# Kernel optimization log

Measured on AMD Instinct MI355X. Metric: run time of the kernel, lower is better.

The kernel has to match this reference:

```python
import jax, jax.numpy as jnp
import numpy as np

EPS = 1e-5
NUM_HEADS = 8
TOP_K = 4

def _ln(x, s, b):
    m = x.mean(-1, keepdims=True)
    v = ((x - m) ** 2).mean(-1, keepdims=True)
    return (x - m) / jnp.sqrt(v + EPS) * s + b

def _mha(x, wq, bq, wk, bk, wv, bv, wo, bo):
    B, S, D = x.shape
    dh = D // NUM_HEADS
    q = (x @ wq + bq).reshape(B, S, NUM_HEADS, dh)
    k = (x @ wk + bk).reshape(B, S, NUM_HEADS, dh)
    v = (x @ wv + bv).reshape(B, S, NUM_HEADS, dh)
    att = jnp.einsum('bqhd,bkhd->bhqk', q, k) / np.sqrt(dh).astype(x.dtype)
    a = jax.nn.softmax(att, axis=-1)
    o = jnp.einsum('bhqk,bkhd->bqhd', a, v).reshape(B, S, D)
    return o @ wo + bo

def _moe(x, rd, ru, w1, b1, w2, b2, ws1, bs1, ws2, bs2):
    B, S, D = x.shape
    N = B * S
    E = ru.shape[-1]
    t = x.reshape(N, D)
    scores = (t @ rd) @ ru                       # [N,E] low-rank router
    probs = jax.nn.softmax(scores, axis=-1)
    tv, ti = jax.lax.top_k(probs, TOP_K)          # [N,K]
    tw = tv / tv.sum(-1, keepdims=True)           # renormalized gate weights
    oh = jax.nn.one_hot(ti, E, dtype=t.dtype)     # [N,K,E]
    gates = (oh * tw[..., None]).sum(1)           # sparse [N,E] combine weights
    h = jax.nn.gelu(jnp.einsum('nd,edh->enh', t, w1) + b1[:, None, :])
    eo = jnp.einsum('enh,ehd->end', h, w2) + b2[:, None, :]
    routed = jnp.einsum('end,ne->nd', eo, gates)
    shared = jax.nn.gelu(t @ ws1 + bs1) @ ws2 + bs2
    out = (routed + shared).reshape(B, S, D)
    # aux losses: load-balance + router z-loss
    f = oh.sum(1).mean(0)                         # mean assignments per expert
    P = probs.mean(0)
    lb = (E / TOP_K) * jnp.sum(f * P)
    z = jnp.mean(jax.nn.logsumexp(scores, axis=-1) ** 2)
    return out, lb, z

def reference(x, ln1_s, ln1_b, ln2_s, ln2_b, wq, bq, wk, bk, wv, bv, wo, bo,
              router_down, router_up, w1, b1, w2, b2, ws1, bs1, ws2, bs2, fn_s, fn_b):
    L = wq.shape[0]
    lbs, zs = [], []
    for l in range(L):
        x = x + _mha(_ln(x, ln1_s[l], ln1_b[l]), wq[l], bq[l], wk[l], bk[l],
                     wv[l], bv[l], wo[l], bo[l])
        moe_out, lb, z = _moe(_ln(x, ln2_s[l], ln2_b[l]), router_down[l], router_up[l],
                              w1[l], b1[l], w2[l], b2[l], ws1[l], bs1[l], ws2[l], bs2[l])
        x = x + moe_out
        lbs.append(lb)
        zs.append(z)
    x = _ln(x, fn_s, fn_b)
    return x, jnp.stack(lbs), jnp.stack(zs)

def setup_inputs() -> dict:
    key = jax.random.key(0)
    ks = jax.random.split(key, 16)
    L, D, E, R, H, HS, B, S = 2, 512, 32, 64, 512, 4096, 4, 1024
    w = 0.02  # init scale for weights
    return {
        'x': jax.random.normal(ks[0], (B, S, D), jnp.float32),
        'ln1_s': jnp.ones((L, D)), 'ln1_b': jnp.zeros((L, D)),
        'ln2_s': jnp.ones((L, D)), 'ln2_b': jnp.zeros((L, D)),
        'wq': jax.random.normal(ks[1], (L, D, D)) * w, 'bq': jnp.zeros((L, D)),
        'wk': jax.random.normal(ks[2], (L, D, D)) * w, 'bk': jnp.zeros((L, D)),
        'wv': jax.random.normal(ks[3], (L, D, D)) * w, 'bv': jnp.zeros((L, D)),
        'wo': jax.random.normal(ks[4], (L, D, D)) * w, 'bo': jnp.zeros((L, D)),
        'router_down': jax.random.normal(ks[5], (L, D, R)) * w,
        'router_up': jax.random.normal(ks[6], (L, R, E)) * w,
        'w1': jax.random.normal(ks[7], (L, E, D, H)) * w, 'b1': jnp.zeros((L, E, H)),
        'w2': jax.random.normal(ks[8], (L, E, H, D)) * w, 'b2': jnp.zeros((L, E, D)),
        'ws1': jax.random.normal(ks[9], (L, D, HS)) * w, 'bs1': jnp.zeros((L, HS)),
        'ws2': jax.random.normal(ks[10], (L, HS, D)) * w, 'bs2': jnp.zeros((L, D)),
        'fn_s': jnp.ones((D,)), 'fn_b': jnp.zeros((D,)),
    }
```

## Files before the change

### kernel.cpp

```cpp
#include <hip/hip_runtime.h>
#include <math.h>

#define NTOK    4096
#define DMODEL  512
#define NEXP    32
#define RRANK   64
#define HEXP    512
#define HSHARED 4096
#define SEQ     1024
#define BATCH   4
#define NHEAD   8
#define TOPK    4
#define NLAYER  2
#define QBLK    64
#define KBLK    64
#define MAXTILE 160
#define DDU     262144

typedef __attribute__((ext_vector_type(8))) short bf16x8;
typedef __attribute__((ext_vector_type(4))) float f32x4;

__device__ __forceinline__ float gelu_f(float x) {
    float t = tanhf(0.7978845608028654f * (x + 0.044715f * x * x * x));
    return 0.5f * x * (1.f + t);
}
__device__ __forceinline__ unsigned short f2bf(float f) {
    unsigned int u = __float_as_uint(f);
    u += 0x7FFFu + ((u >> 16) & 1u);
    return (unsigned short)(u >> 16);
}
__device__ __forceinline__ float bf2f(unsigned short u) {
    return __uint_as_float((unsigned int)u << 16);
}
__device__ __forceinline__ void gl_lds16(const void* g, void* l) {
    __builtin_amdgcn_global_load_lds(
        (const __attribute__((address_space(1))) void*)g,
        (__attribute__((address_space(3))) void*)l, 16, 0, 0);
}

__device__ __forceinline__ void ln_body(const float* x, const float* s, const float* b,
                                        unsigned short* outb, int rowblk) {
    int wave = threadIdx.x >> 6, lane = threadIdx.x & 63;
    int row = rowblk * 4 + wave;
    const float* xr = x + (size_t)row * DMODEL;
    float v[8];
    float sum = 0.f;
#pragma unroll
    for (int i = 0; i < 8; i++) { v[i] = xr[lane + i * 64]; sum += v[i]; }
#pragma unroll
    for (int o = 32; o; o >>= 1) sum += __shfl_xor(sum, o);
    float m = sum * (1.f / DMODEL);
    float vs = 0.f;
#pragma unroll
    for (int i = 0; i < 8; i++) { float d = v[i] - m; vs += d * d; }
#pragma unroll
    for (int o = 32; o; o >>= 1) vs += __shfl_xor(vs, o);
    float rstd = rsqrtf(vs * (1.f / DMODEL) + 1e-5f);
#pragma unroll
    for (int i = 0; i < 8; i++) {
        int c = lane + i * 64;
        outb[(size_t)row * DMODEL + c] = f2bf((v[i] - m) * rstd * s[c] + b[c]);
    }
}

template <int SK, bool MOE, int MODE, bool ROUTER = false>
__global__ __launch_bounds__(256) void reduceln_kernel(
    const float* __restrict__ pbuf, const float* __restrict__ bias,
    const unsigned short* __restrict__ eogb, const float* __restrict__ topw,
    const int* __restrict__ pos, float* __restrict__ xb,
    const float* __restrict__ s, const float* __restrict__ b,
    float* __restrict__ outf, unsigned short* __restrict__ outb,
    const float* __restrict__ rdru, float* __restrict__ rsc) {
    int wave = threadIdx.x >> 6, lane = threadIdx.x & 63;
    int row = blockIdx.x * 4 + wave;
    int cb = lane * 8;
    size_t base = (size_t)row * DMODEL + cb;
    float v[8];
    {
        float4 a0 = *(const float4*)(xb + base);
        float4 a1 = *(const float4*)(xb + base + 4);
        float4 b0 = *(const float4*)(bias + cb);
        float4 b1 = *(const float4*)(bias + cb + 4);
        v[0] = a0.x + b0.x; v[1] = a0.y + b0.y; v[2] = a0.z + b0.z; v[3] = a0.w + b0.w;
        v[4] = a1.x + b1.x; v[5] = a1.y + b1.y; v[6] = a1.z + b1.z; v[7] = a1.w + b1.w;
    }
#pragma unroll
    for (int sk = 0; sk < SK; sk++) {
        const float* p = pbuf + (size_t)sk * NTOK * DMODEL + base;
        float4 p0 = *(const float4*)p;
        float4 p1 = *(const float4*)(p + 4);
        v[0] += p0.x; v[1] += p0.y; v[2] += p0.z; v[3] += p0.w;
        v[4] += p1.x; v[5] += p1.y; v[6] += p1.z; v[7] += p1.w;
    }
    if (MOE) {
#pragma unroll
        for (int k = 0; k < TOPK; k++) {
            float w = topw[row * TOPK + k];
            bf16x8 e = *(const bf16x8*)(eogb + (size_t)pos[row * TOPK + k] * DMODEL + cb);
#pragma unroll
            for (int i = 0; i < 8; i++) v[i] += w * bf2f((unsigned short)e[i]);
        }
    }
    *(float4*)(xb + base) = make_float4(v[0], v[1], v[2], v[3]);
    *(float4*)(xb + base + 4) = make_float4(v[4], v[5], v[6], v[7]);
    float sum = 0.f;
#pragma unroll
    for (int i = 0; i < 8; i++) sum += v[i];
#pragma unroll
    for (int o = 32; o; o >>= 1) sum += __shfl_xor(sum, o);
    float m = sum * (1.f / DMODEL);
    float vs = 0.f;
#pragma unroll
    for (int i = 0; i < 8; i++) { float d = v[i] - m; vs += d * d; }
#pragma unroll
    for (int o = 32; o; o >>= 1) vs += __shfl_xor(vs, o);
    float rstd = rsqrtf(vs * (1.f / DMODEL) + 1e-5f);
    float rr[8];
#pragma unroll
    for (int i = 0; i < 8; i++) {
        int c = cb + i;
        rr[i] = (v[i] - m) * rstd * s[c] + b[c];
        if (MODE != 1) outf[(size_t)row * DMODEL + c] = rr[i];
        if (MODE != 0) outb[(size_t)row * DMODEL + c] = f2bf(rr[i]);
    }
    if (ROUTER) {
        float sc[NEXP];
#pragma unroll
        for (int e = 0; e < NEXP; e++) sc[e] = 0.f;
#pragma unroll
        for (int i = 0; i < 8; i++) {
            const float4* rp = (const float4*)(rdru + (size_t)(cb + i) * NEXP);
            float rv = rr[i];
#pragma unroll
            for (int e4 = 0; e4 < 8; e4++) {
                float4 q = rp[e4];
                sc[e4 * 4 + 0] += rv * q.x;
                sc[e4 * 4 + 1] += rv * q.y;
                sc[e4 * 4 + 2] += rv * q.z;
                sc[e4 * 4 + 3] += rv * q.w;
            }
        }
#pragma unroll
        for (int e = 0; e < NEXP; e++) {
#pragma unroll
            for (int o = 32; o; o >>= 1) sc[e] += __shfl_xor(sc[e], o);
        }
        if (lane == 0) {
            float* rp = rsc + (size_t)row * NEXP;
#pragma unroll
            for (int e = 0; e < NEXP; e++) rp[e] = sc[e];
        }
    }
}

__device__ __forceinline__ void wt_tile_body(char* ldsraw, const float* src,
                                             unsigned short* dst, int K, int N,
                                             int tx, int ty) {
    float (*tbuf)[68] = (float(*)[68])ldsraw;
    int tid = threadIdx.x;
    int k0 = ty * 64, n0 = tx * 64;
    int r = tid >> 2, cb4 = (tid & 3) * 4;
#pragma unroll
    for (int i = 0; i < 4; i++)
        *(float4*)&tbuf[r][cb4 + i * 16] = *(const float4*)(src + (size_t)(k0 + r) * N + n0 + cb4 + i * 16);
    __syncthreads();
    int g = tid & 7, nr = tid >> 3;
#pragma unroll
    for (int i = 0; i < 2; i++) {
        int n = nr + i * 32;
        bf16x8 v;
#pragma unroll
        for (int j = 0; j < 8; j++) v[j] = (short)f2bf(tbuf[g * 8 + j][n]);
        *(bf16x8*)(dst + (size_t)(n0 + n) * K + k0 + g * 8) = v;
    }
}

__device__ __forceinline__ void rdru_tile_body(char* ldsraw, const float* A,
                                               const float* W, float* C, int m0) {
    float (*Asf)[68] = (float(*)[68])ldsraw;
    float (*Wsf)[68] = (float(*)[68])(ldsraw + 4352);
    int tid = threadIdx.x;
    int ml = tid >> 2, kl = (tid & 3) << 2;
    const float* aptr = A + (size_t)(m0 + ml) * RRANK + kl;
    int kr = tid >> 4, nc = (tid & 15) << 2;
    bool wvalid = nc < NEXP;
    const float* wptr = W + (size_t)kr * NEXP + nc;
    int tm = (tid >> 4) << 2, tn = (tid & 15) << 2;
    float acc[4][4] = {{0.f}};
    for (int k0 = 0; k0 < RRANK; k0 += 16) {
        float4 av = *(const float4*)(aptr + k0);
        float4 wv = make_float4(0.f, 0.f, 0.f, 0.f);
        if (wvalid) wv = *(const float4*)(wptr + (size_t)k0 * NEXP);
        Asf[kl + 0][ml] = av.x; Asf[kl + 1][ml] = av.y;
        Asf[kl + 2][ml] = av.z; Asf[kl + 3][ml] = av.w;
        *(float4*)&Wsf[kr][nc] = wv;
        __syncthreads();
#pragma unroll
        for (int kk = 0; kk < 16; kk++) {
            float4 a4 = *(const float4*)&Asf[kk][tm];
            float4 w4 = *(const float4*)&Wsf[kk][tn];
            acc[0][0] += a4.x * w4.x; acc[0][1] += a4.x * w4.y; acc[0][2] += a4.x * w4.z; acc[0][3] += a4.x * w4.w;
            acc[1][0] += a4.y * w4.x; acc[1][1] += a4.y * w4.y; acc[1][2] += a4.y * w4.z; acc[1][3] += a4.y * w4.w;
            acc[2][0] += a4.z * w4.x; acc[2][1] += a4.z * w4.y; acc[2][2] += a4.z * w4.z; acc[2][3] += a4.z * w4.w;
            acc[3][0] += a4.w * w4.x; acc[3][1] += a4.w * w4.y; acc[3][2] += a4.w * w4.z; acc[3][3] += a4.w * w4.w;
        }
        __syncthreads();
    }
#pragma unroll
    for (int i = 0; i < 4; i++) {
        float* crow = C + (size_t)(m0 + tm + i) * NEXP;
#pragma unroll
        for (int j = 0; j < 4; j++) {
            int nn = tn + j;
            if (nn < NEXP) crow[nn] = acc[i][j];
        }
    }
}

__global__ __launch_bounds__(256) void prep0_kernel(
    const float* __restrict__ wq, const float* __restrict__ wk, const float* __restrict__ wv,
    const float* __restrict__ bq, const float* __restrict__ bk, const float* __restrict__ bv,
    unsigned short* __restrict__ wqkvt, float* __restrict__ bqkv, int* __restrict__ stats,
    const float* __restrict__ rdw, const float* __restrict__ ruw, float* __restrict__ rdru,
    const float* __restrict__ xb, const float* __restrict__ ln1_s, const float* __restrict__ ln1_b,
    unsigned short* __restrict__ hb) {
    __shared__ char lds[17408];
    int bkid = blockIdx.x;
    int tid = threadIdx.x;
    if (bkid < 192) {
        int w = bkid >> 6, t = bkid & 63;
        const float* src = (w == 0) ? wq : (w == 1 ? wk : wv);
        wt_tile_body(lds, src, wqkvt + (size_t)w * DDU, 512, 512, t & 7, t >> 3);
    } else if (bkid < 198) {
        int i = (bkid - 192) * 256 + tid;
        float val = (i < 512) ? bq[i] : (i < 1024 ? bk[i - 512] : bv[i - 1024]);
        bqkv[i] = val;
        if (i < 160) stats[i] = 0;
    } else if (bkid < 206) {
        rdru_tile_body(lds, rdw, ruw, rdru, (bkid - 198) * 64);
    } else {
        ln_body(xb, ln1_s, ln1_b, hb, bkid - 206);
    }
}

__global__ __launch_bounds__(256) void vtr_kernel(const unsigned short* __restrict__ QKV,
                                                  unsigned short* __restrict__ Vt) {
    int st = blockIdx.x, hh = blockIdx.y, bb = blockIdx.z;
    __shared__ unsigned short t[64][72];
    int r = threadIdx.x >> 3, g = threadIdx.x & 7;
#pragma unroll
    for (int i = 0; i < 2; i++) {
        int row = r + i * 32;
        bf16x8 v = *(const bf16x8*)(QKV + (size_t)(bb * SEQ + st * 64 + row) * 1536 + 1024 + hh * 64 + g * 8);
        *(bf16x8*)&t[row][g * 8] = v;
    }
    __syncthreads();
#pragma unroll
    for (int i = 0; i < 2; i++) {
        int d = r + i * 32;
        bf16x8 v;
#pragma unroll
        for (int j = 0; j < 8; j++) v[j] = (short)t[g * 8 + j][d];
        *(bf16x8*)(Vt + (size_t)((bb * NHEAD + hh) * 64 + d) * SEQ + st * 64 + g * 8) = v;
    }
}

template <bool GELU, bool GATHER, bool EXPERT, bool OUTBF16, int SK>
__device__ __forceinline__ void gemm_body(
    char* asb, char* bsb,
    unsigned int rb, unsigned int gx, unsigned int tot, int zidx,
    const unsigned short* Ab, const unsigned short* Wt,
    const float* bias, void* Cvoid, int M, int Nn, int Kk,
    const int* rowmap, const int* cntp, const int* offp, const int* tinfo) {
    constexpr int RS  = 128;
    constexpr int CH  = 8;
    constexpr int RPI = 8;
    constexpr int AIW = 4;
    constexpr int BIW = 2;
    unsigned int lg = (rb & 7) * (tot >> 3) + (rb >> 3);
    unsigned int bx = lg % gx;
    unsigned int by = lg / gx;
    int n0 = bx * 64;
    int m0;
    size_t cbase = 0;
    int kbeg = 0, kend = Kk;
    if (EXPERT) {
        int t = by;
        if (t >= tinfo[0]) return;
        int e = tinfo[1 + 2 * t];
        m0 = tinfo[2 + 2 * t];
        M = cntp[e];
        Wt += (size_t)e * Nn * Kk;
        bias += (size_t)e * Nn;
        int oe = offp[e];
        cbase = (size_t)oe * Nn;
        if (GATHER) rowmap += oe;
        else Ab += (size_t)oe * Kk;
    } else {
        m0 = by * 128;
    }
    if (SK > 1) {
        int chunk = Kk / SK;
        kbeg = zidx * chunk;
        kend = kbeg + chunk;
        cbase = (size_t)zidx * M * Nn;
    }
    int tid = threadIdx.x;
    int wave = tid >> 6, lane = tid & 63;
    int wm = wave >> 1, wn = wave & 1;
    int l15 = lane & 15, l16 = lane >> 4;
    int c16 = lane & (CH - 1);
    int ro  = lane / CH;

    const char* aptr[AIW];
    const char* bptr[BIW];
#pragma unroll
    for (int j = 0; j < AIW; j++) {
        int rloc = j * RPI + ro;
        int row = wave * 32 + rloc;
        int grow = m0 + row;
        int arow = GATHER ? rowmap[grow] : grow;
        int srcoff = ((c16 ^ (rloc & (CH - 1))) << 4);
        aptr[j] = (const char*)Ab + (((size_t)arow * Kk) << 1) + srcoff;
    }
#pragma unroll
    for (int j = 0; j < BIW; j++) {
        int rloc = j * RPI + ro;
        int row = wave * 16 + rloc;
        int srcoff = ((c16 ^ (rloc & (CH - 1))) << 4);
        bptr[j] = (const char*)Wt + (((size_t)(n0 + row) * Kk) << 1) + srcoff;
    }

    f32x4 acc[4][2];
#pragma unroll
    for (int m = 0; m < 4; m++)
#pragma unroll
        for (int n = 0; n < 2; n++)
#pragma unroll
            for (int j = 0; j < 4; j++) acc[m][n][j] = 0.f;

    for (int k0 = kbeg; k0 < kend; k0 += 64) {
        size_t kb = (size_t)k0 << 1;
#pragma unroll
        for (int j = 0; j < AIW; j++) gl_lds16(aptr[j] + kb, asb + wave * 32 * RS + j * 1024);
#pragma unroll
        for (int j = 0; j < BIW; j++) gl_lds16(bptr[j] + kb, bsb + wave * 16 * RS + j * 1024);
        __syncthreads();
#pragma unroll
        for (int kk = 0; kk < 2; kk++) {
            int k8 = kk * 4 + l16;
            bf16x8 a[4], b[2];
#pragma unroll
            for (int m = 0; m < 4; m++) {
                int row = wm * 64 + m * 16 + l15;
                a[m] = *(const bf16x8*)(asb + row * RS + ((k8 * 16) ^ ((row & (CH - 1)) << 4)));
            }
#pragma unroll
            for (int n = 0; n < 2; n++) {
                int row = wn * 32 + n * 16 + l15;
                b[n] = *(const bf16x8*)(bsb + row * RS + ((k8 * 16) ^ ((row & (CH - 1)) << 4)));
            }
#pragma unroll
            for (int m = 0; m < 4; m++)
#pragma unroll
                for (int n = 0; n < 2; n++)
                    acc[m][n] = __builtin_amdgcn_mfma_f32_16x16x32_bf16(a[m], b[n], acc[m][n], 0, 0, 0);
        }
        __syncthreads();
    }

#pragma unroll
    for (int m = 0; m < 4; m++) {
#pragma unroll
        for (int n = 0; n < 2; n++) {
            int col = n0 + wn * 32 + n * 16 + l15;
            float bv = (SK == 1 && bias) ? bias[col] : 0.f;
#pragma unroll
            for (int j = 0; j < 4; j++) {
                int row = m0 + wm * 64 + m * 16 + l16 * 4 + j;
                if (row >= M) continue;
                float val = acc[m][n][j] + bv;
                if (SK == 1 && GELU) val = gelu_f(val);
                if (SK == 1 && OUTBF16)
                    ((unsigned short*)Cvoid)[cbase + (size_t)row * Nn + col] = f2bf(val);
                else
                    ((float*)Cvoid)[cbase + (size_t)row * Nn + col] = val;
            }
        }
    }
}

template <int RIDER>
__global__ __launch_bounds__(256, 2) void qkv_kernel(
    const unsigned short* __restrict__ hb, const unsigned short* __restrict__ wqkvt,
    const float* __restrict__ bqkv, unsigned short* __restrict__ qkv_bf,
    const float* __restrict__ srcA, const float* __restrict__ srcB,
    unsigned short* __restrict__ dstA, unsigned short* __restrict__ dstB,
    int* __restrict__ stats) {
    __shared__ char lds[24576];
    unsigned int bid = blockIdx.x;
    if (bid < 768) {
        gemm_body<false, false, false, true, 1>(
            lds, lds + 16384, bid, 24, 768, 0,
            hb, wqkvt, bqkv, qkv_bf, NTOK, 1536, DMODEL, nullptr, nullptr, nullptr, nullptr);
    } else if (RIDER == 0) {
        int t = bid - 768;
        wt_tile_body(lds, srcA, dstA, 512, 512, t & 7, t >> 3);
    } else {
        unsigned int eb = bid - 768;
        if (eb < 2048) {
            int e = eb >> 6, tt = eb & 63;
            wt_tile_body(lds, srcA + (size_t)e * DDU, dstA + (size_t)e * DDU,
                         512, 512, tt & 7, tt >> 3);
        } else if (eb < 2560) {
            int t = eb - 2048;
            wt_tile_body(lds, srcB, dstB, 4096, 512, t & 7, t >> 3);
        } else {
            if (threadIdx.x < 160) stats[threadIdx.x] = 0;
        }
    }
}

__device__ __forceinline__ void attn_body(char* lds, unsigned int bid,
                                          const unsigned short* QKV,
                                          const unsigned short* Vt,
                                          unsigned short* O) {
    int qt = bid & 15, hh = (bid >> 4) & 7, bb = bid >> 7;
    char* Qs = lds;
    char* Ks = lds + 8192;
    char* Vs = lds + 16384;
    char* Ps = lds + 24576;
    int tid = threadIdx.x;
    int w = tid >> 6, l = tid & 63;
    int l15 = l & 15, l16 = l >> 4;

    {
        int r = tid >> 3, g = tid & 7;
        const unsigned short* qbase = QKV + (size_t)(bb * SEQ + qt * QBLK) * 1536 + hh * 64;
#pragma unroll
        for (int i = 0; i < 2; i++) {
            int row = r + i * 32;
            bf16x8 v = *(const bf16x8*)(qbase + (size_t)row * 1536 + g * 8);
            *(bf16x8*)(Qs + row * 128 + ((g * 16) ^ ((row & 7) << 4))) = v;
        }
    }
    f32x4 accO[4];
#pragma unroll
    for (int n = 0; n < 4; n++)
#pragma unroll
        for (int j = 0; j < 4; j++) accO[n][j] = 0.f;
    float m_r[4] = {-1e30f, -1e30f, -1e30f, -1e30f};
    float l_r[4] = {0.f, 0.f, 0.f, 0.f};

    const unsigned short* kbase = QKV + (size_t)(bb * SEQ) * 1536 + 512 + hh * 64;
    const unsigned short* vbase = Vt + (size_t)((bb * NHEAD + hh) * 64) * SEQ;

    for (int kt = 0; kt < SEQ / KBLK; kt++) {
        __syncthreads();
        {
            int r = tid >> 3, g = tid & 7;
#pragma unroll
            for (int i = 0; i < 2; i++) {
                int row = r + i * 32;
                bf16x8 kv = *(const bf16x8*)(kbase + (size_t)(kt * KBLK + row) * 1536 + g * 8);
                *(bf16x8*)(Ks + row * 128 + ((g * 16) ^ ((row & 7) << 4))) = kv;
                bf16x8 vv = *(const bf16x8*)(vbase + (size_t)row * SEQ + kt * KBLK + g * 8);
                *(bf16x8*)(Vs + row * 128 + ((g * 16) ^ ((row & 7) << 4))) = vv;
            }
        }
        __syncthreads();
        f32x4 s_acc[4];
#pragma unroll
        for (int n = 0; n < 4; n++)
#pragma unroll
            for (int j = 0; j < 4; j++) s_acc[n][j] = 0.f;
#pragma unroll
        for (int st = 0; st < 2; st++) {
            int kb = st * 64 + l16 * 16;
            int qrow = w * 16 + l15;
            bf16x8 a = *(const bf16x8*)(Qs + qrow * 128 + (kb ^ ((qrow & 7) << 4)));
#pragma unroll
            for (int n = 0; n < 4; n++) {
                int kr = n * 16 + l15;
                bf16x8 b = *(const bf16x8*)(Ks + kr * 128 + (kb ^ ((kr & 7) << 4)));
                s_acc[n] = __builtin_amdgcn_mfma_f32_16x16x32_bf16(a, b, s_acc[n], 0, 0, 0);
            }
        }
        char* pw = Ps + w * 2048;
#pragma unroll
        for (int j = 0; j < 4; j++) {
            float s0 = s_acc[0][j] * 0.125f, s1 = s_acc[1][j] * 0.125f;
            float s2 = s_acc[2][j] * 0.125f, s3 = s_acc[3][j] * 0.125f;
            float tmax = fmaxf(fmaxf(s0, s1), fmaxf(s2, s3));
#pragma unroll
            for (int o = 1; o < 16; o <<= 1) tmax = fmaxf(tmax, __shfl_xor(tmax, o));
            float mnew = fmaxf(m_r[j], tmax);
            float resc = __expf(m_r[j] - mnew);
            float p0 = __expf(s0 - mnew), p1 = __expf(s1 - mnew);
            float p2 = __expf(s2 - mnew), p3 = __expf(s3 - mnew);
            float ps = p0 + p1 + p2 + p3;
#pragma unroll
            for (int o = 1; o < 16; o <<= 1) ps += __shfl_xor(ps, o);
            l_r[j] = l_r[j] * resc + ps;
            m_r[j] = mnew;
            accO[0][j] *= resc; accO[1][j] *= resc;
            accO[2][j] *= resc; accO[3][j] *= resc;
            int prow = l16 * 4 + j;
            int sw = (prow & 7) << 4;
            *(unsigned short*)(pw + prow * 128 + ((2 * l15) ^ sw)) = f2bf(p0);
            *(unsigned short*)(pw + prow * 128 + ((2 * l15 + 32) ^ sw)) = f2bf(p1);
            *(unsigned short*)(pw + prow * 128 + ((2 * l15 + 64) ^ sw)) = f2bf(p2);
            *(unsigned short*)(pw + prow * 128 + ((2 * l15 + 96) ^ sw)) = f2bf(p3);
        }
#pragma unroll
        for (int st = 0; st < 2; st++) {
            int kb = st * 64 + l16 * 16;
            bf16x8 pa = *(const bf16x8*)(pw + l15 * 128 + (kb ^ ((l15 & 7) << 4)));
#pragma unroll
            for (int n = 0; n < 4; n++) {
                int vr = n * 16 + l15;
                bf16x8 vb = *(const bf16x8*)(Vs + vr * 128 + (kb ^ ((vr & 7) << 4)));
                accO[n] = __builtin_amdgcn_mfma_f32_16x16x32_bf16(pa, vb, accO[n], 0, 0, 0);
            }
        }
    }
    unsigned short* obase = O + (size_t)(bb * SEQ + qt * QBLK + w * 16) * DMODEL + hh * 64;
#pragma unroll
    for (int j = 0; j < 4; j++) {
        float inv = 1.f / l_r[j];
        int row = l16 * 4 + j;
#pragma unroll
        for (int n = 0; n < 4; n++)
            obase[(size_t)row * DMODEL + n * 16 + l15] = f2bf(accO[n][j] * inv);
    }
}

template <int RIDER>
__global__ __launch_bounds__(256, 2) void attn_kernel(
    const unsigned short* __restrict__ QKV, const unsigned short* __restrict__ Vt,
    unsigned short* __restrict__ O,
    const float* __restrict__ w1src, const float* __restrict__ ws1src,
    unsigned short* __restrict__ w1t, unsigned short* __restrict__ ws1t) {
    __shared__ char lds[32768];
    unsigned int bid = blockIdx.x;
    if (bid < 512) {
        attn_body(lds, bid, QKV, Vt, O);
    } else if (RIDER == 0) {
        unsigned int eb = bid - 512;
        if (eb < 2048) {
            int e = eb >> 6, tt = eb & 63;
            wt_tile_body(lds, w1src + (size_t)e * DDU, w1t + (size_t)e * DDU,
                         512, 512, tt & 7, tt >> 3);
        } else {
            int t = eb - 2048;
            wt_tile_body(lds, ws1src, ws1t, 512, 4096, t & 63, t >> 6);
        }
    }
}

template <int RIDER>
__global__ __launch_bounds__(256, 2) void op_kernel(
    const unsigned short* __restrict__ t1b, const unsigned short* __restrict__ wot,
    float* __restrict__ pbuf,
    const float* __restrict__ w2src, const float* __restrict__ ws2src,
    unsigned short* __restrict__ w2t, unsigned short* __restrict__ ws2t) {
    __shared__ char lds[24576];
    unsigned int bid = blockIdx.x;
    if (bid < 512) {
        gemm_body<false, false, false, false, 2>(
            lds, lds + 16384, bid & 255, 8, 256, bid >> 8,
            t1b, wot, nullptr, pbuf, NTOK, DMODEL, DMODEL, nullptr, nullptr, nullptr, nullptr);
    } else if (RIDER == 0) {
        unsigned int eb = bid - 512;
        if (eb < 2048) {
            int e = eb >> 6, tt = eb & 63;
            wt_tile_body(lds, w2src + (size_t)e * DDU, w2t + (size_t)e * DDU,
                         512, 512, tt & 7, tt >> 3);
        } else {
            int t = eb - 2048;
            wt_tile_body(lds, ws2src, ws2t, 4096, 512, t & 7, t >> 3);
        }
    }
}

__global__ __launch_bounds__(256, 2) void mlp1_kernel(
    const unsigned short* __restrict__ hb,
    const unsigned short* __restrict__ ws1t, const float* __restrict__ bs1,
    unsigned short* __restrict__ hidb,
    const unsigned short* __restrict__ w1t, const float* __restrict__ b1,
    unsigned short* __restrict__ ehid,
    const int* __restrict__ perm, const int* __restrict__ cnt,
    const int* __restrict__ poff, const int* __restrict__ tinfo,
    const float* __restrict__ nwq, const float* __restrict__ nwk,
    const float* __restrict__ nwv, const float* __restrict__ nwo,
    const float* __restrict__ nbq, const float* __restrict__ nbk, const float* __restrict__ nbv,
    unsigned short* __restrict__ wqkvt, unsigned short* __restrict__ wot,
    float* __restrict__ bqkv,
    const float* __restrict__ nrdw, const float* __restrict__ nruw, float* __restrict__ rdru) {
    __shared__ char lds[24576];
    unsigned int bid = blockIdx.x;
    if (bid < 2048) {
        gemm_body<true, false, false, true, 1>(
            lds, lds + 16384, bid, 64, 2048, 0,
            hb, ws1t, bs1, hidb, NTOK, HSHARED, DMODEL, nullptr, nullptr, nullptr, nullptr);
    } else if (bid < 3328) {
        gemm_body<true, true, true, true, 1>(
            lds, lds + 16384, bid - 2048, 8, 1280, 0,
            hb, w1t, b1, ehid, 0, HEXP, DMODEL, perm, cnt, poff, tinfo);
    } else {
        unsigned int eb = bid - 3328;
        if (eb < 256) {
            int w = eb >> 6, t = eb & 63;
            const float* src; unsigned short* dst;
            if (w == 0)      { src = nwq; dst = wqkvt; }
            else if (w == 1) { src = nwk; dst = wqkvt + DDU; }
            else if (w == 2) { src = nwv; dst = wqkvt + 2 * (size_t)DDU; }
            else             { src = nwo; dst = wot; }
            wt_tile_body(lds, src, dst, 512, 512, t & 7, t >> 3);
        } else if (eb < 262) {
            int i = (eb - 256) * 256 + threadIdx.x;
            float val = (i < 512) ? nbq[i] : (i < 1024 ? nbk[i - 512] : nbv[i - 1024]);
            bqkv[i] = val;
        } else {
            rdru_tile_body(lds, nrdw, nruw, rdru, (eb - 262) * 64);
        }
    }
}

__global__ __launch_bounds__(256, 2) void mlp2_kernel(
    const unsigned short* __restrict__ hidb,
    const unsigned short* __restrict__ ws2t, float* __restrict__ pbuf,
    const unsigned short* __restrict__ ehid,
    const unsigned short* __restrict__ w2t, const float* __restrict__ b2,
    unsigned short* __restrict__ eogb,
    const int* __restrict__ cnt, const int* __restrict__ poff,
    const int* __restrict__ tinfo,
    const float* __restrict__ nw1, const float* __restrict__ nws1,
    unsigned short* __restrict__ w1t, unsigned short* __restrict__ ws1t) {
    __shared__ char lds[24576];
    unsigned int bid = blockIdx.x;
    if (bid < 1024) {
        int zidx = bid >> 8;
        gemm_body<false, false, false, false, 4>(
            lds, lds + 16384, bid & 255, 8, 256, zidx,
            hidb, ws2t, nullptr, pbuf, NTOK, DMODEL, HSHARED, nullptr, nullptr, nullptr, nullptr);
    } else if (bid < 2304) {
        gemm_body<false, false, true, true, 1>(
            lds, lds + 16384, bid - 1024, 8, 1280, 0,
            ehid, w2t, b2, eogb, 0, DMODEL, HEXP, nullptr, cnt, poff, tinfo);
    } else {
        unsigned int eb = bid - 2304;
        if (eb < 2048) {
            int e = eb >> 6, tt = eb & 63;
            wt_tile_body(lds, nw1 + (size_t)e * DDU, w1t + (size_t)e * DDU,
                         512, 512, tt & 7, tt >> 3);
        } else {
            int t = eb - 2048;
            wt_tile_body(lds, nws1, ws1t, 512, 4096, t & 63, t >> 6);
        }
    }
}

__global__ __launch_bounds__(256) void router_topk(const float* __restrict__ rsc,
                                                   float* __restrict__ topw,
                                                   int* __restrict__ topi,
                                                   int* __restrict__ cnt,
                                                   float* __restrict__ sumP,
                                                   float* __restrict__ zacc) {
    __shared__ float wP[4][NEXP];
    __shared__ int wC[4][NEXP];
    __shared__ float wZ[4];
    int tid = threadIdx.x;
    int wv = tid >> 6, lane = tid & 63;
    int n = blockIdx.x * 256 + tid;
    float sc[NEXP];
    float mx = -1e30f;
#pragma unroll
    for (int e = 0; e < NEXP; e++) { sc[e] = rsc[n * NEXP + e]; mx = fmaxf(mx, sc[e]); }
    float se = 0.f;
#pragma unroll
    for (int e = 0; e < NEXP; e++) { sc[e] = expf(sc[e] - mx); se += sc[e]; }
    float invse = 1.f / se;
    float lse = mx + logf(se);
    float z = lse * lse;
#pragma unroll
    for (int o = 32; o; o >>= 1) z += __shfl_xor(z, o);
    if (lane == 0) wZ[wv] = z;
#pragma unroll
    for (int e = 0; e < NEXP; e++) {
        float pv = sc[e] * invse;
#pragma unroll
        for (int o = 32; o; o >>= 1) pv += __shfl_xor(pv, o);
        if (lane == 0) wP[wv][e] = pv;
    }
    float tv[TOPK]; int ti[TOPK];
#pragma unroll
    for (int k = 0; k < TOPK; k++) {
        float best = -1.f; int bi = 0;
#pragma unroll
        for (int e = 0; e < NEXP; e++) {
            if (sc[e] > best) { best = sc[e]; bi = e; }
        }
        tv[k] = best * invse; ti[k] = bi; sc[bi] = -1.f;
    }
    float s4 = tv[0] + tv[1] + tv[2] + tv[3];
#pragma unroll
    for (int k = 0; k < TOPK; k++) {
        topw[n * TOPK + k] = tv[k] / s4;
        topi[n * TOPK + k] = ti[k];
    }
#pragma unroll
    for (int e = 0; e < NEXP; e++) {
        unsigned long long b0 = __ballot(ti[0] == e);
        unsigned long long b1 = __ballot(ti[1] == e);
        unsigned long long b2 = __ballot(ti[2] == e);
        unsigned long long b3 = __ballot(ti[3] == e);
        if (lane == 0)
            wC[wv][e] = __popcll(b0) + __popcll(b1) + __popcll(b2) + __popcll(b3);
    }
    __syncthreads();
    if (tid < NEXP) {
        atomicAdd(&sumP[tid], wP[0][tid] + wP[1][tid] + wP[2][tid] + wP[3][tid]);
        atomicAdd(&cnt[tid], wC[0][tid] + wC[1][tid] + wC[2][tid] + wC[3][tid]);
    }
    if (tid == 0) atomicAdd(zacc, wZ[0] + wZ[1] + wZ[2] + wZ[3]);
}

__global__ void scanaux_kernel(const int* __restrict__ cnt, int* __restrict__ poff,
                               int* __restrict__ tinfo, int* __restrict__ perm,
                               const float* __restrict__ sumP, const float* __restrict__ zacc,
                               float* __restrict__ out_aux, int l) {
    int lane = threadIdx.x;
    int c = (lane < NEXP) ? cnt[lane] : 0;
    int nt = (c + 127) >> 7;
    int x = nt;
#pragma unroll
    for (int o = 1; o < 32; o <<= 1) {
        int y = __shfl_up(x, o);
        if (lane >= o) x += y;
    }
    int excl = x - nt;
    if (lane < NEXP) {
        poff[lane] = excl * 128;
        for (int i = 0; i < nt; i++) {
            tinfo[1 + 2 * (excl + i)] = lane;
            tinfo[2 + 2 * (excl + i)] = i * 128;
        }
        for (int i = c; i < nt * 128; i++) perm[excl * 128 + i] = 0;
    }
    float lb = (lane < NEXP) ? ((float)c / (float)NTOK) * (sumP[lane] / (float)NTOK) : 0.f;
#pragma unroll
    for (int o = 32; o; o >>= 1) lb += __shfl_xor(lb, o);
    if (lane == 31) {
        tinfo[0] = x;
        out_aux[l] = lb * (float)NEXP / (float)TOPK;
        out_aux[NLAYER + l] = zacc[0] / (float)NTOK;
    }
}

__global__ __launch_bounds__(256) void scatter_kernel(const int* __restrict__ topi,
                                                      const int* __restrict__ poff,
                                                      int* __restrict__ cursor,
                                                      int* __restrict__ perm,
                                                      int* __restrict__ pos) {
    __shared__ int lcnt[NEXP];
    __shared__ int lbase[NEXP];
    if (threadIdx.x < NEXP) lcnt[threadIdx.x] = 0;
    __syncthreads();
    int i = blockIdx.x * 256 + threadIdx.x;
    int e = topi[i];
    int lr = atomicAdd(&lcnt[e], 1);
    __syncthreads();
    if (threadIdx.x < NEXP && lcnt[threadIdx.x] > 0)
        lbase[threadIdx.x] = atomicAdd(&cursor[threadIdx.x], lcnt[threadIdx.x]);
    __syncthreads();
    int g = poff[e] + lbase[e] + lr;
    perm[g] = i >> 2;
    pos[i] = g;
}

extern "C" void kernel_launch(void* const* d_in, const int* in_sizes, int n_in,
                              void* d_out, int out_size, void* d_ws, size_t ws_size,
                              hipStream_t stream) {
    (void)in_sizes; (void)n_in; (void)out_size; (void)ws_size;
    const float* x_in  = (const float*)d_in[0];
    const float* ln1_s = (const float*)d_in[1];
    const float* ln1_b = (const float*)d_in[2];
    const float* ln2_s = (const float*)d_in[3];
    const float* ln2_b = (const float*)d_in[4];
    const float* wq = (const float*)d_in[5];
    const float* bq = (const float*)d_in[6];
    const float* wk = (const float*)d_in[7];
    const float* bk = (const float*)d_in[8];
    const float* wv = (const float*)d_in[9];
    const float* bv = (const float*)d_in[10];
    const float* wo = (const float*)d_in[11];
    const float* bo = (const float*)d_in[12];
    const float* rdw = (const float*)d_in[13];
    const float* ruw = (const float*)d_in[14];
    const float* w1 = (const float*)d_in[15];
    const float* b1 = (const float*)d_in[16];
    const float* w2 = (const float*)d_in[17];
    const float* b2 = (const float*)d_in[18];
    const float* ws1 = (const float*)d_in[19];
    const float* bs1 = (const float*)d_in[20];
    const float* ws2 = (const float*)d_in[21];
    const float* bs2 = (const float*)d_in[22];
    const float* fn_s = (const float*)d_in[23];
    const float* fn_b = (const float*)d_in[24];

    float* ws = (float*)d_ws;
    const size_t ND = (size_t)NTOK * DMODEL;
    const size_t PADROWS = (size_t)MAXTILE * 128;
    size_t o = 0;
    float* xb  = ws + o; o += ND;
    unsigned short* hb     = (unsigned short*)(ws + o); o += ND / 2;
    unsigned short* qkv_bf = (unsigned short*)(ws + o); o += (size_t)NTOK * 1536 / 2;
    unsigned short* vT     = (unsigned short*)(ws + o); o += ND / 2;
    unsigned short* t1b    = (unsigned short*)(ws + o); o += ND / 2;
    unsigned short* hidb   = (unsigned short*)(ws + o); o += (size_t)NTOK * HSHARED / 2;
    unsigned short* ehid   = (unsigned short*)(ws + o); o += PADROWS * HEXP / 2;
    unsigned short* eogb   = (unsigned short*)(ws + o); o += PADROWS * DMODEL / 2;
    float* pbuf = ws + o; o += 4 * ND;
    float* rdru = ws + o; o += (size_t)DMODEL * NEXP;
    float* rsc  = ws + o; o += (size_t)NTOK * NEXP;
    float* topw = ws + o; o += (size_t)NTOK * TOPK;
    float* bqkv = ws + o; o += 1536;
    int* topi = (int*)(ws + o); o += (size_t)NTOK * TOPK;
    int* pos  = (int*)(ws + o); o += (size_t)NTOK * TOPK;
    int* perm = (int*)(ws + o); o += PADROWS;
    int* stats = (int*)(ws + o); o += 256;
    int* tinfo = (int*)(ws + o); o += 512;
    int* cnt = stats;
    int* cursor = stats + 32;
    int* poff = stats + 64;
    float* sumP = (float*)(stats + 96);
    float* zacc = sumP + 32;
    unsigned short* wbf = (unsigned short*)(ws + o);
    unsigned short* wqkvt = wbf;
    unsigned short* wot  = wqkvt + 3 * (size_t)DDU;
    unsigned short* w1t  = wot + DDU;
    unsigned short* w2t  = w1t + (size_t)NEXP * DDU;
    unsigned short* ws1t = w2t + (size_t)NEXP * DDU;
    unsigned short* ws2t = ws1t + (size_t)DMODEL * HSHARED;

    float* out_x = (float*)d_out;
    float* out_aux = out_x + ND;

    hipMemcpyAsync(xb, x_in, ND * sizeof(float), hipMemcpyDeviceToDevice, stream);

    dim3 blk(256);

    for (int l = 0; l < NLAYER; l++) {
        const size_t DD = (size_t)DMODEL * DMODEL;
        bool hasNext = (l + 1 < NLAYER);
        int lnx = hasNext ? (l + 1) : l;
        if (l == 0) {
            prep0_kernel<<<1230, blk, 0, stream>>>(
                wq, wk, wv, bq, bk, bv, wqkvt, bqkv, stats,
                rdw, ruw, rdru, xb, ln1_s, ln1_b, hb);
            qkv_kernel<0><<<832, blk, 0, stream>>>(
                hb, wqkvt, bqkv, qkv_bf, wo, nullptr, wot, nullptr, nullptr);
        } else {
            qkv_kernel<1><<<3329, blk, 0, stream>>>(
                hb, wqkvt, bqkv, qkv_bf,
                w2 + (size_t)l * NEXP * DD, ws2 + (size_t)l * HSHARED * DMODEL,
                w2t, ws2t, stats);
        }
        vtr_kernel<<<dim3(SEQ / 64, NHEAD, BATCH), blk, 0, stream>>>(qkv_bf, vT);
        if (l == 0)
            attn_kernel<0><<<3072, blk, 0, stream>>>(qkv_bf, vT, t1b, w1, ws1, w1t, ws1t);
        else
            attn_kernel<1><<<512, blk, 0, stream>>>(qkv_bf, vT, t1b, nullptr, nullptr, nullptr, nullptr);
        if (l == 0)
            op_kernel<0><<<3072, blk, 0, stream>>>(t1b, wot, pbuf, w2, ws2, w2t, ws2t);
        else
            op_kernel<1><<<512, blk, 0, stream>>>(t1b, wot, pbuf, nullptr, nullptr, nullptr, nullptr);
        reduceln_kernel<2, false, 1, true><<<NTOK / 4, blk, 0, stream>>>(
            pbuf, bo + l * DMODEL, nullptr, nullptr, nullptr, xb,
            ln2_s + l * DMODEL, ln2_b + l * DMODEL, nullptr, hb, rdru, rsc);
        router_topk<<<NTOK / 256, blk, 0, stream>>>(rsc, topw, topi, cnt, sumP, zacc);
        scanaux_kernel<<<1, 64, 0, stream>>>(cnt, poff, tinfo, perm, sumP, zacc, out_aux, l);
        scatter_kernel<<<NTOK * TOPK / 256, blk, 0, stream>>>(topi, poff, cursor, perm, pos);
        int ln1g = hasNext ? 3598 : 3328;
        mlp1_kernel<<<ln1g, blk, 0, stream>>>(
            hb, ws1t, bs1 + (size_t)l * HSHARED, hidb,
            w1t, b1 + (size_t)l * NEXP * HEXP, ehid,
            perm, cnt, poff, tinfo,
            wq + (size_t)lnx * DD, wk + (size_t)lnx * DD,
            wv + (size_t)lnx * DD, wo + (size_t)lnx * DD,
            bq + (size_t)lnx * DMODEL, bk + (size_t)lnx * DMODEL, bv + (size_t)lnx * DMODEL,
            wqkvt, wot, bqkv,
            rdw + (size_t)lnx * DMODEL * RRANK, ruw + (size_t)lnx * RRANK * NEXP, rdru);
        int ln2g = hasNext ? 4864 : 2304;
        mlp2_kernel<<<ln2g, blk, 0, stream>>>(
            hidb, ws2t, pbuf,
            ehid, w2t, b2 + (size_t)l * NEXP * DMODEL, eogb,
            cnt, poff, tinfo,
            w1 + (size_t)lnx * NEXP * DD, ws1 + (size_t)lnx * DMODEL * HSHARED,
            w1t, ws1t);
        if (hasNext) {
            reduceln_kernel<4, true, 1, false><<<NTOK / 4, blk, 0, stream>>>(
                pbuf, bs2 + l * DMODEL, eogb, topw, pos, xb,
                ln1_s + (l + 1) * DMODEL, ln1_b + (l + 1) * DMODEL, nullptr, hb, nullptr, nullptr);
        } else {
            reduceln_kernel<4, true, 0, false><<<NTOK / 4, blk, 0, stream>>>(
                pbuf, bs2 + l * DMODEL, eogb, topw, pos, xb,
                fn_s, fn_b, out_x, nullptr, nullptr, nullptr);
        }
    }
}
```

Measured before the change: 507.9 us.

## Fuse V transpose into attention load and scan into router via last-block

Removes the separate V-transpose kernel. Attention now reads V rows straight from the QKV buffer and scatters them transposed into swizzled LDS. It also folds the single-block scan/aux kernel into router_topk using a last-block-done atomic counter. Both changes cut two kernel launches per layer and the extra global round trip for Vt, at the cost of scalar 2-byte LDS stores in the attention inner loop. The done counter sits in the stats area and must be zeroed each layer; that depends on existing stats resets covering index 129.

```diff
diff --git a/kernel.cpp b/kernel.cpp
--- a/kernel.cpp
+++ b/kernel.cpp
@@ -240,28 +240,6 @@
         rdru_tile_body(lds, rdw, ruw, rdru, (bkid - 198) * 64);
     } else {
         ln_body(xb, ln1_s, ln1_b, hb, bkid - 206);
-    }
-}
-
-__global__ __launch_bounds__(256) void vtr_kernel(const unsigned short* __restrict__ QKV,
-                                                  unsigned short* __restrict__ Vt) {
-    int st = blockIdx.x, hh = blockIdx.y, bb = blockIdx.z;
-    __shared__ unsigned short t[64][72];
-    int r = threadIdx.x >> 3, g = threadIdx.x & 7;
-#pragma unroll
-    for (int i = 0; i < 2; i++) {
-        int row = r + i * 32;
-        bf16x8 v = *(const bf16x8*)(QKV + (size_t)(bb * SEQ + st * 64 + row) * 1536 + 1024 + hh * 64 + g * 8);
-        *(bf16x8*)&t[row][g * 8] = v;
-    }
-    __syncthreads();
-#pragma unroll
-    for (int i = 0; i < 2; i++) {
-        int d = r + i * 32;
-        bf16x8 v;
-#pragma unroll
-        for (int j = 0; j < 8; j++) v[j] = (short)t[g * 8 + j][d];
-        *(bf16x8*)(Vt + (size_t)((bb * NHEAD + hh) * 64 + d) * SEQ + st * 64 + g * 8) = v;
     }
 }
 
@@ -423,7 +401,6 @@
 
 __device__ __forceinline__ void attn_body(char* lds, unsigned int bid,
                                           const unsigned short* QKV,
-                                          const unsigned short* Vt,
                                           unsigned short* O) {
     int qt = bid & 15, hh = (bid >> 4) & 7, bb = bid >> 7;
     char* Qs = lds;
@@ -453,7 +430,7 @@
     float l_r[4] = {0.f, 0.f, 0.f, 0.f};
 
     const unsigned short* kbase = QKV + (size_t)(bb * SEQ) * 1536 + 512 + hh * 64;
-    const unsigned short* vbase = Vt + (size_t)((bb * NHEAD + hh) * 64) * SEQ;
+    const unsigned short* vbase = QKV + (size_t)(bb * SEQ) * 1536 + 1024 + hh * 64;
 
     for (int kt = 0; kt < SEQ / KBLK; kt++) {
         __syncthreads();
@@ -464,8 +441,14 @@
                 int row = r + i * 32;
                 bf16x8 kv = *(const bf16x8*)(kbase + (size_t)(kt * KBLK + row) * 1536 + g * 8);
                 *(bf16x8*)(Ks + row * 128 + ((g * 16) ^ ((row & 7) << 4))) = kv;
-                bf16x8 vv = *(const bf16x8*)(vbase + (size_t)row * SEQ + kt * KBLK + g * 8);
-                *(bf16x8*)(Vs + row * 128 + ((g * 16) ^ ((row & 7) << 4))) = vv;
+                bf16x8 vv = *(const bf16x8*)(vbase + (size_t)(kt * KBLK + row) * 1536 + g * 8);
+#pragma unroll
+                for (int j = 0; j < 8; j++) {
+                    int jj = (j + g) & 7;
+                    int d = g * 8 + jj;
+                    *(unsigned short*)(Vs + d * 128 + ((2 * row) ^ (jj << 4))) =
+                        (unsigned short)vv[jj];
+                }
             }
         }
         __syncthreads();
@@ -537,14 +520,13 @@
 
 template <int RIDER>
 __global__ __launch_bounds__(256, 2) void attn_kernel(
-    const unsigned short* __restrict__ QKV, const unsigned short* __restrict__ Vt,
-    unsigned short* __restrict__ O,
+    const unsigned short* __restrict__ QKV, unsigned short* __restrict__ O,
     const float* __restrict__ w1src, const float* __restrict__ ws1src,
     unsigned short* __restrict__ w1t, unsigned short* __restrict__ ws1t) {
     __shared__ char lds[32768];
     unsigned int bid = blockIdx.x;
     if (bid < 512) {
-        attn_body(lds, bid, QKV, Vt, O);
+        attn_body(lds, bid, QKV, O);
     } else if (RIDER == 0) {
         unsigned int eb = bid - 512;
         if (eb < 2048) {
@@ -666,10 +648,16 @@
                                                    int* __restrict__ topi,
                                                    int* __restrict__ cnt,
                                                    float* __restrict__ sumP,
-                                                   float* __restrict__ zacc) {
+                                                   float* __restrict__ zacc,
+                                                   int* __restrict__ done,
+                                                   int* __restrict__ poff,
+                                                   int* __restrict__ tinfo,
+                                                   int* __restrict__ perm,
+                                                   float* __restrict__ out_aux, int l) {
     __shared__ float wP[4][NEXP];
     __shared__ int wC[4][NEXP];
     __shared__ float wZ[4];
+    __shared__ int amLast;
     int tid = threadIdx.x;
     int wv = tid >> 6, lane = tid & 63;
     int n = blockIdx.x * 256 + tid;
@@ -724,37 +712,39 @@
         atomicAdd(&cnt[tid], wC[0][tid] + wC[1][tid] + wC[2][tid] + wC[3][tid]);
     }
     if (tid == 0) atomicAdd(zacc, wZ[0] + wZ[1] + wZ[2] + wZ[3]);
-}
-
-__global__ void scanaux_kernel(const int* __restrict__ cnt, int* __restrict__ poff,
-                               int* __restrict__ tinfo, int* __restrict__ perm,
-                               const float* __restrict__ sumP, const float* __restrict__ zacc,
-                               float* __restrict__ out_aux, int l) {
-    int lane = threadIdx.x;
-    int c = (lane < NEXP) ? cnt[lane] : 0;
-    int nt = (c + 127) >> 7;
-    int x = nt;
-#pragma unroll
-    for (int o = 1; o < 32; o <<= 1) {
-        int y = __shfl_up(x, o);
-        if (lane >= o) x += y;
-    }
-    int excl = x - nt;
-    if (lane < NEXP) {
-        poff[lane] = excl * 128;
-        for (int i = 0; i < nt; i++) {
-            tinfo[1 + 2 * (excl + i)] = lane;
-            tinfo[2 + 2 * (excl + i)] = i * 128;
-        }
-        for (int i = c; i < nt * 128; i++) perm[excl * 128 + i] = 0;
-    }
-    float lb = (lane < NEXP) ? ((float)c / (float)NTOK) * (sumP[lane] / (float)NTOK) : 0.f;
-#pragma unroll
-    for (int o = 32; o; o >>= 1) lb += __shfl_xor(lb, o);
-    if (lane == 31) {
-        tinfo[0] = x;
-        out_aux[l] = lb * (float)NEXP / (float)TOPK;
-        out_aux[NLAYER + l] = zacc[0] / (float)NTOK;
+    __syncthreads();
+    __threadfence();
+    if (tid == 0) amLast = (atomicAdd(done, 1) == (int)gridDim.x - 1);
+    __syncthreads();
+    if (amLast && tid < 64) {
+        __threadfence();
+        int laneid = tid;
+        int c = (laneid < NEXP) ? atomicAdd(&cnt[laneid], 0) : 0;
+        int nt = (c + 127) >> 7;
+        int x = nt;
+#pragma unroll
+        for (int o = 1; o < 32; o <<= 1) {
+            int y = __shfl_up(x, o);
+            if (laneid >= o) x += y;
+        }
+        int excl = x - nt;
+        if (laneid < NEXP) {
+            poff[laneid] = excl * 128;
+            for (int i = 0; i < nt; i++) {
+                tinfo[1 + 2 * (excl + i)] = laneid;
+                tinfo[2 + 2 * (excl + i)] = i * 128;
+            }
+            for (int i = c; i < nt * 128; i++) perm[excl * 128 + i] = 0;
+        }
+        float sp = (laneid < NEXP) ? atomicAdd(&sumP[laneid], 0.f) : 0.f;
+        float lb = (laneid < NEXP) ? ((float)c / (float)NTOK) * (sp / (float)NTOK) : 0.f;
+#pragma unroll
+        for (int o = 32; o; o >>= 1) lb += __shfl_xor(lb, o);
+        if (laneid == 31) {
+            tinfo[0] = x;
+            out_aux[l] = lb * (float)NEXP / (float)TOPK;
+            out_aux[NLAYER + l] = atomicAdd(zacc, 0.f) / (float)NTOK;
+        }
     }
 }
 
@@ -816,7 +806,6 @@
     float* xb  = ws + o; o += ND;
     unsigned short* hb     = (unsigned short*)(ws + o); o += ND / 2;
     unsigned short* qkv_bf = (unsigned short*)(ws + o); o += (size_t)NTOK * 1536 / 2;
-    unsigned short* vT     = (unsigned short*)(ws + o); o += ND / 2;
     unsigned short* t1b    = (unsigned short*)(ws + o); o += ND / 2;
     unsigned short* hidb   = (unsigned short*)(ws + o); o += (size_t)NTOK * HSHARED / 2;
     unsigned short* ehid   = (unsigned short*)(ws + o); o += PADROWS * HEXP / 2;
@@ -836,6 +825,7 @@
     int* poff = stats + 64;
     float* sumP = (float*)(stats + 96);
     float* zacc = sumP + 32;
+    int* done = stats + 129;
     unsigned short* wbf = (unsigned short*)(ws + o);
     unsigned short* wqkvt = wbf;
     unsigned short* wot  = wqkvt + 3 * (size_t)DDU;
@@ -867,11 +857,10 @@
                 w2 + (size_t)l * NEXP * DD, ws2 + (size_t)l * HSHARED * DMODEL,
                 w2t, ws2t, stats);
         }
-        vtr_kernel<<<dim3(SEQ / 64, NHEAD, BATCH), blk, 0, stream>>>(qkv_bf, vT);
         if (l == 0)
-            attn_kernel<0><<<3072, blk, 0, stream>>>(qkv_bf, vT, t1b, w1, ws1, w1t, ws1t);
+            attn_kernel<0><<<3072, blk, 0, stream>>>(qkv_bf, t1b, w1, ws1, w1t, ws1t);
         else
-            attn_kernel<1><<<512, blk, 0, stream>>>(qkv_bf, vT, t1b, nullptr, nullptr, nullptr, nullptr);
+            attn_kernel<1><<<512, blk, 0, stream>>>(qkv_bf, t1b, nullptr, nullptr, nullptr, nullptr);
         if (l == 0)
             op_kernel<0><<<3072, blk, 0, stream>>>(t1b, wot, pbuf, w2, ws2, w2t, ws2t);
         else
@@ -879,8 +868,8 @@
         reduceln_kernel<2, false, 1, true><<<NTOK / 4, blk, 0, stream>>>(
             pbuf, bo + l * DMODEL, nullptr, nullptr, nullptr, xb,
             ln2_s + l * DMODEL, ln2_b + l * DMODEL, nullptr, hb, rdru, rsc);
-        router_topk<<<NTOK / 256, blk, 0, stream>>>(rsc, topw, topi, cnt, sumP, zacc);
-        scanaux_kernel<<<1, 64, 0, stream>>>(cnt, poff, tinfo, perm, sumP, zacc, out_aux, l);
+        router_topk<<<NTOK / 256, blk, 0, stream>>>(
+            rsc, topw, topi, cnt, sumP, zacc, done, poff, tinfo, perm, out_aux, l);
         scatter_kernel<<<NTOK * TOPK / 256, blk, 0, stream>>>(topi, poff, cursor, perm, pos);
         int ln1g = hasNext ? 3598 : 3328;
         mlp1_kernel<<<ln1g, blk, 0, stream>>>(
```

Result: slower. 536.8 us (+5.7%).
